# Kernel optimization log

Hardware: AMD Instinct MI355X
Metric: run time of the kernel (lower is better)

Reference implementation:

```python
import jax, jax.numpy as jnp
import numpy as np

F = 128          # num_features
NRBF = 20        # num_rbf_features
N_NODES = 25000
N_EDGES = 400000


def setup_inputs() -> dict:
    key = jax.random.key(0)
    ks = jax.random.split(key, 12)
    inp = {
        "idx_i": jax.random.randint(ks[0], (N_EDGES,), 0, N_NODES, dtype=jnp.int32),
        "idx_j": jax.random.randint(ks[1], (N_EDGES,), 0, N_NODES, dtype=jnp.int32),
        "rel_dir": jax.random.normal(ks[2], (N_EDGES, 3), dtype=jnp.float32),
        "rel_dist_cut": jax.random.uniform(ks[3], (N_EDGES,), dtype=jnp.float32),
        "rbf_features": jax.random.normal(ks[4], (N_EDGES, NRBF), dtype=jnp.float32),
        "scalar_features": jax.random.normal(ks[5], (N_NODES, F), dtype=jnp.float32),
        "vector_features": jax.random.normal(ks[6], (N_NODES, F, 3), dtype=jnp.float32),
        # scalar_network: Linear(F,F) -> SiLU -> Linear(F,3F)
        "W1": jax.random.normal(ks[7], (F, F), dtype=jnp.float32) / np.sqrt(F),
        "b1": jnp.zeros((F,), dtype=jnp.float32),
        "W2": jax.random.normal(ks[8], (3 * F, F), dtype=jnp.float32) / np.sqrt(F),
        "b2": jnp.zeros((3 * F,), dtype=jnp.float32),
        # rbf_network: Linear(NRBF, 3F)
        "Wr": jax.random.normal(ks[9], (3 * F, NRBF), dtype=jnp.float32) / np.sqrt(NRBF),
        "br": jnp.zeros((3 * F,), dtype=jnp.float32),
    }
    return inp


def reference(idx_i, idx_j, rel_dir, rel_dist_cut, rbf_features,
              scalar_features, vector_features, W1, b1, W2, b2, Wr, br):
    n_nodes = scalar_features.shape[0]
    # phi: per-node MLP -> [N, 3F]
    h = jax.nn.silu(scalar_features @ W1.T + b1)
    phi = h @ W2.T + b2
    # W: RBF-derived edge weights gated by cosine-cut distance -> [E, 3F]
    W = (rbf_features @ Wr.T + br) * rel_dist_cut[:, None]
    phi_W = phi[idx_j] * W                                  # [E, 3F]
    phi_W_vv, phi_W_ss, phi_W_vs = jnp.split(phi_W, 3, axis=-1)
    # scatter-add scalar residuals
    scalar_res = jax.ops.segment_sum(phi_W_ss, idx_i, num_segments=n_nodes)
    # per-edge vector messages [E, F, 3]
    vec_per_edge = (vector_features[idx_j] * phi_W_vv[..., None]
                    + phi_W_vs[..., None] * rel_dir[:, None, :])
    vector_res = jax.ops.segment_sum(vec_per_edge, idx_i, num_segments=n_nodes)
    return scalar_features + scalar_res, vector_features + vector_res
```

## Files before the change

### kernel.cpp

```cpp
#include <hip/hip_runtime.h>
#include <hip/hip_fp16.h>

#define F 128
#define F3 384
#define NRBF 20
#define NPB 16
#define CHUNK 64

typedef unsigned int u32;
typedef _Float16 half8 __attribute__((ext_vector_type(8)));
typedef float floatx4 __attribute__((ext_vector_type(4)));

__device__ __forceinline__ float2 uph(u32 u) {
    __half2 h = *(__half2*)&u;
    return __half22float2(h);
}
__device__ __forceinline__ u32 pkh(float a, float b) {
    __half2 h = __floats2half2_rn(a, b);
    return *(u32*)&h;
}

__global__ void prep_kernel(const float* __restrict__ Wr,
                            const float* __restrict__ W1, const float* __restrict__ W2,
                            u32* __restrict__ WrTh, _Float16* __restrict__ Wh,
                            int* __restrict__ counts, int n_nodes) {
    int t = blockIdx.x * blockDim.x + threadIdx.x;
    if (t < 10 * F3) {
        int rr = t / F3, f = t % F3;
        WrTh[rr * F3 + f] = pkh(Wr[f * NRBF + 2 * rr], Wr[f * NRBF + 2 * rr + 1]);
        return;
    }
    int u = t - 10 * F3;
    if (u < (F + F3) * F) {
        int n = u >> 7, k = u & (F - 1);
        float w = (n < F) ? W1[n * F + k] : W2[(size_t)(n - F) * F + k];
        Wh[u] = (_Float16)w;
        return;
    }
    int z = u - (F + F3) * F;
    if (z < n_nodes) counts[z] = 0;
}

__launch_bounds__(256)
__global__ void phi_mfma_kernel(const float* __restrict__ sf,
                                const _Float16* __restrict__ Wh,
                                const float* __restrict__ b1, const float* __restrict__ b2,
                                __half* __restrict__ gbufh, int n_nodes) {
    __shared__ _Float16 hl[4][16][136];
    int tid = threadIdx.x;
    int lane = tid & 63;
    int wv = tid >> 6;
    int col = lane & 15;
    int kg = lane >> 4;
    int row0 = blockIdx.x * 64 + wv * 16;

    half8 a1[4];
#pragma unroll
    for (int kb = 0; kb < 4; kb++) {
        int rr = row0 + col;
        if (rr >= n_nodes) rr = n_nodes - 1;
        const float4* xp = (const float4*)(sf + (size_t)rr * F + kb * 32 + kg * 8);
        float4 x0 = xp[0], x1 = xp[1];
        half8 a;
        a[0] = (_Float16)x0.x; a[1] = (_Float16)x0.y; a[2] = (_Float16)x0.z; a[3] = (_Float16)x0.w;
        a[4] = (_Float16)x1.x; a[5] = (_Float16)x1.y; a[6] = (_Float16)x1.z; a[7] = (_Float16)x1.w;
        a1[kb] = a;
    }

    floatx4 acc[8];
#pragma unroll
    for (int nt = 0; nt < 8; nt++) acc[nt] = (floatx4){0.f, 0.f, 0.f, 0.f};
#pragma unroll
    for (int nt = 0; nt < 8; nt++) {
#pragma unroll
        for (int kb = 0; kb < 4; kb++) {
            half8 b = *(const half8*)(Wh + (size_t)(nt * 16 + col) * F + kb * 32 + kg * 8);
            acc[nt] = __builtin_amdgcn_mfma_f32_16x16x32_f16(a1[kb], b, acc[nt], 0, 0, 0);
        }
    }
#pragma unroll
    for (int nt = 0; nt < 8; nt++) {
        int f1 = nt * 16 + col;
        float bb = b1[f1];
#pragma unroll
        for (int r = 0; r < 4; r++) {
            float v = acc[nt][r] + bb;
            float s = v / (1.f + __expf(-v));
            hl[wv][kg * 4 + r][f1] = (_Float16)s;
        }
    }

    half8 a2[4];
#pragma unroll
    for (int kb = 0; kb < 4; kb++)
        a2[kb] = *(const half8*)&hl[wv][col][kb * 32 + kg * 8];

#pragma unroll
    for (int c = 0; c < 3; c++) {
#pragma unroll
        for (int nt = 0; nt < 8; nt++) acc[nt] = (floatx4){0.f, 0.f, 0.f, 0.f};
#pragma unroll
        for (int nt = 0; nt < 8; nt++) {
#pragma unroll
            for (int kb = 0; kb < 4; kb++) {
                half8 b = *(const half8*)(Wh + (size_t)(F + c * 128 + nt * 16 + col) * F + kb * 32 + kg * 8);
                acc[nt] = __builtin_amdgcn_mfma_f32_16x16x32_f16(a2[kb], b, acc[nt], 0, 0, 0);
            }
        }
#pragma unroll
        for (int nt = 0; nt < 8; nt++) {
            int f2 = c * 128 + nt * 16 + col;
            float bb = b2[f2];
            int slot = (f2 & 63) * 12 + ((f2 >> 6) & 1) * 6 + (f2 >> 7);
#pragma unroll
            for (int r = 0; r < 4; r++) {
                int node = row0 + kg * 4 + r;
                if (node < n_nodes)
                    gbufh[(size_t)node * 768 + slot] = __float2half(acc[nt][r] + bb);
            }
        }
    }
}

__launch_bounds__(256)
__global__ void fusedC_kernel(const int* __restrict__ idx_i, int* __restrict__ counts,
                              const float* __restrict__ vf, __half* __restrict__ gbufh,
                              int n_nodes, int n_edges, int HB) {
    int blk = blockIdx.x, tid = threadIdx.x;
    if (blk < HB) {
        int e = blk * 256 + tid;
        if (e < n_edges) atomicAdd(&counts[idx_i[e]], 1);
    } else {
        int idx = (blk - HB) * 256 + tid;
        int node = idx >> 6, lane = idx & 63;
        if (node < n_nodes) {
            const float* v = vf + (size_t)node * F3;
            __half* g = gbufh + (size_t)node * 768 + lane * 12;
            g[3]  = __float2half(v[lane * 3 + 0]);
            g[4]  = __float2half(v[lane * 3 + 1]);
            g[5]  = __float2half(v[lane * 3 + 2]);
            g[9]  = __float2half(v[(lane + 64) * 3 + 0]);
            g[10] = __float2half(v[(lane + 64) * 3 + 1]);
            g[11] = __float2half(v[(lane + 64) * 3 + 2]);
        }
    }
}

#define SCAN_T 1024
#define SCAN_MAXN 25600
__launch_bounds__(SCAN_T)
__global__ void scan_lds_kernel(const int* __restrict__ counts, int* __restrict__ row_start,
                                int* __restrict__ cursor, int n) {
    __shared__ int sbuf[SCAN_MAXN];
    __shared__ int partial[SCAN_T];
    int t = threadIdx.x;
    for (int i = t; i < n; i += SCAN_T) sbuf[i] = counts[i];
    __syncthreads();
    int C = (n + SCAN_T - 1) / SCAN_T;
    int beg = t * C, end = min(beg + C, n);
    int sum = 0;
    for (int i = beg; i < end; i++) sum += sbuf[i];
    partial[t] = sum;
    __syncthreads();
    for (int off = 1; off < SCAN_T; off <<= 1) {
        int v = (t >= off) ? partial[t - off] : 0;
        __syncthreads();
        partial[t] += v;
        __syncthreads();
    }
    int base = (t == 0) ? 0 : partial[t - 1];
    for (int i = beg; i < end; i++) { int c = sbuf[i]; sbuf[i] = base; base += c; }
    __syncthreads();
    for (int i = t; i < n; i += SCAN_T) { int v = sbuf[i]; row_start[i] = v; cursor[i] = v; }
    if (t == SCAN_T - 1) row_start[n] = partial[SCAN_T - 1];
}

__launch_bounds__(1024)
__global__ void scan_kernel(const int* __restrict__ counts, int* __restrict__ row_start,
                            int* __restrict__ cursor, int n) {
    __shared__ int partial[1024];
    int t = threadIdx.x;
    int C = (n + 1023) / 1024;
    int beg = t * C, end = min(beg + C, n);
    int sum = 0;
    for (int i = beg; i < end; i++) sum += counts[i];
    partial[t] = sum;
    __syncthreads();
    for (int off = 1; off < 1024; off <<= 1) {
        int v = (t >= off) ? partial[t - off] : 0;
        __syncthreads();
        partial[t] += v;
        __syncthreads();
    }
    int base = (t == 0) ? 0 : partial[t - 1];
    for (int i = beg; i < end; i++) {
        int c = counts[i];
        row_start[i] = base; cursor[i] = base; base += c;
    }
    if (t == 1023) row_start[n] = partial[1023];
}

__global__ void build_records(const int* __restrict__ idx_i, const int* __restrict__ idx_j,
                              const float* __restrict__ rel_dir, const float* __restrict__ rdc,
                              const float* __restrict__ rbf, int* __restrict__ cursor,
                              u32* __restrict__ recs, int n_edges) {
    int e = blockIdx.x * blockDim.x + threadIdx.x;
    if (e >= n_edges) return;
    int p = atomicAdd(&cursor[idx_i[e]], 1);
    u32 r[16];
    r[0] = (u32)idx_j[e];
    r[1] = __float_as_uint(rdc[e]);
    r[2] = __float_as_uint(rel_dir[e * 3 + 0]);
    r[3] = __float_as_uint(rel_dir[e * 3 + 1]);
    r[4] = __float_as_uint(rel_dir[e * 3 + 2]);
    const float* rb = rbf + (size_t)e * NRBF;
#pragma unroll
    for (int t = 0; t < 10; t++) r[5 + t] = pkh(rb[2 * t], rb[2 * t + 1]);
    r[15] = 0;
    float4* dst = (float4*)(recs + (size_t)p * 16);
    const float4* src = (const float4*)r;
    dst[0] = src[0]; dst[1] = src[1]; dst[2] = src[2]; dst[3] = src[3];
}

__global__ void scatter_kernel(const int* __restrict__ idx_i, int* __restrict__ cursor,
                               int* __restrict__ edge_order, int n_edges) {
    int e = blockIdx.x * blockDim.x + threadIdx.x;
    if (e < n_edges) {
        int p = atomicAdd(&cursor[idx_i[e]], 1);
        edge_order[p] = e;
    }
}

__launch_bounds__(256)
__global__ void gather4_kernel(const float* __restrict__ sf, const float* __restrict__ vf,
                               const u32* __restrict__ WrTh, const float* __restrict__ br,
                               const u32* __restrict__ gbuf, const u32* __restrict__ recs,
                               const int* __restrict__ row_start,
                               float* __restrict__ out_s, float* __restrict__ out_v,
                               int n_nodes) {
    __shared__ u32 lsm[4][CHUNK * 16];
    int tid = threadIdx.x;
    int lane = tid & 63;
    int wvid = tid >> 6;
    int w = wvid & 1;
    int node = blockIdx.x * 2 + (wvid >> 1);
    if (node >= n_nodes) return;
    u32* lds = lsm[wvid];

    int fb = lane + 64 * w;
    u32 wrpk[3][10];
    float brv[3];
#pragma unroll
    for (int k = 0; k < 3; k++) {
        brv[k] = br[fb + 128 * k];
#pragma unroll
        for (int rr = 0; rr < 10; rr++)
            wrpk[k][rr] = WrTh[rr * F3 + fb + 128 * k];
    }

    float acc_s = 0.f, av0 = 0.f, av1 = 0.f, av2 = 0.f;
    int beg = row_start[node];
    int end = row_start[node + 1];

    for (int cb = beg; cb < end; cb += CHUNK) {
        int cnt = min(CHUNK, end - cb);
        {
            const float4* src = (const float4*)(recs + (size_t)cb * 16);
            int nf4 = cnt * 4;
            for (int t = lane; t < nf4; t += 64)
                ((float4*)lds)[t] = src[t];
        }

        auto issueL = [&](u32& g0, u32& g1, u32& g2, int m) {
            if (m < cnt) {
                int j = (int)lds[m * 16];
                const u32* gp = gbuf + (size_t)j * 384 + lane * 6 + w * 3;
                g0 = gp[0]; g1 = gp[1]; g2 = gp[2];
            }
        };
        auto computeE = [&](u32 g0, u32 g1, u32 g2, int m) {
            const uint4* q = (const uint4*)(lds + m * 16);
            uint4 q0 = q[0], q1 = q[1], q2 = q[2], q3 = q[3];
            float rd = __uint_as_float(q0.y);
            float dx = __uint_as_float(q0.z);
            float dy = __uint_as_float(q0.w);
            float dz = __uint_as_float(q1.x);
            u32 rbu[10] = { q1.y, q1.z, q1.w, q2.x, q2.y, q2.z, q2.w, q3.x, q3.y, q3.z };
            __half2 z2 = __floats2half2_rn(0.f, 0.f);
            __half2 wa0 = z2, wa1 = z2, wa2 = z2;
#pragma unroll
            for (int rr = 0; rr < 10; rr++) {
                __half2 rbh = *(__half2*)&rbu[rr];
                wa0 = __hfma2(rbh, *(__half2*)&wrpk[0][rr], wa0);
                wa1 = __hfma2(rbh, *(__half2*)&wrpk[1][rr], wa1);
                wa2 = __hfma2(rbh, *(__half2*)&wrpk[2][rr], wa2);
            }
            float W0  = __half2float(wa0.x) + __half2float(wa0.y) + brv[0];
            float W1v = __half2float(wa1.x) + __half2float(wa1.y) + brv[1];
            float W2v = __half2float(wa2.x) + __half2float(wa2.y) + brv[2];
            float2 p01  = uph(g0);
            float2 p2v0 = uph(g1);
            float2 v12  = uph(g2);
            float pw0 = W0  * rd * p01.x;
            float pw1 = W1v * rd * p01.y;
            float pw2 = W2v * rd * p2v0.x;
            acc_s += pw1;
            av0 += p2v0.y * pw0 + pw2 * dx;
            av1 += v12.x  * pw0 + pw2 * dy;
            av2 += v12.y  * pw0 + pw2 * dz;
        };

        u32 A0, A1, A2, B0, B1, B2, C0, C1, C2, D0, D1, D2;
        issueL(A0, A1, A2, 0); issueL(B0, B1, B2, 1);
        issueL(C0, C1, C2, 2); issueL(D0, D1, D2, 3);
        int m = 0;
        while (true) {
            if (m >= cnt) break; computeE(A0, A1, A2, m); m++; issueL(A0, A1, A2, m + 3);
            if (m >= cnt) break; computeE(B0, B1, B2, m); m++; issueL(B0, B1, B2, m + 3);
            if (m >= cnt) break; computeE(C0, C1, C2, m); m++; issueL(C0, C1, C2, m + 3);
            if (m >= cnt) break; computeE(D0, D1, D2, m); m++; issueL(D0, D1, D2, m + 3);
        }
    }

    out_s[(size_t)node * F + fb] = sf[(size_t)node * F + fb] + acc_s;
    const float* vfi = vf + (size_t)node * F3 + fb * 3;
    float* ovi = out_v + (size_t)node * F3 + fb * 3;
    ovi[0] = vfi[0] + av0;
    ovi[1] = vfi[1] + av1;
    ovi[2] = vfi[2] + av2;
}

__launch_bounds__(256)
__global__ void gather3_kernel(const int* __restrict__ idx_j,
                               const float* __restrict__ rel_dir, const float* __restrict__ rdc,
                               const float* __restrict__ rbf,
                               const float* __restrict__ sf, const float* __restrict__ vf,
                               const u32* __restrict__ WrTh, const float* __restrict__ br,
                               const u32* __restrict__ gbuf,
                               const int* __restrict__ row_start, const int* __restrict__ edge_order,
                               float* __restrict__ out_s, float* __restrict__ out_v,
                               int n_nodes) {
    int lane = threadIdx.x & 63;
    int w = (threadIdx.x >> 6) & 1;
    int node = blockIdx.x * 2 + (threadIdx.x >> 7);
    if (node >= n_nodes) return;

    int fb = lane + 64 * w;
    u32 wrpk[3][10];
    float brv[3];
#pragma unroll
    for (int k = 0; k < 3; k++) {
        brv[k] = br[fb + 128 * k];
#pragma unroll
        for (int rr = 0; rr < 10; rr++)
            wrpk[k][rr] = WrTh[rr * F3 + fb + 128 * k];
    }

    float acc_s = 0.f, av0 = 0.f, av1 = 0.f, av2 = 0.f;
    int beg = row_start[node];
    int end = row_start[node + 1];

    for (int cb = beg; cb < end; cb += 64) {
        int cnt = min(64, end - cb);
        int jv = 0; float rdv = 0.f, dxv = 0.f, dyv = 0.f, dzv = 0.f;
        u32 rbm[10];
#pragma unroll
        for (int rr = 0; rr < 10; rr++) rbm[rr] = 0;
        if (lane < cnt) {
            int e = edge_order[cb + lane];
            jv = idx_j[e];
            rdv = rdc[e];
            dxv = rel_dir[e * 3 + 0]; dyv = rel_dir[e * 3 + 1]; dzv = rel_dir[e * 3 + 2];
            const float4* rp = (const float4*)(rbf + (size_t)e * NRBF);
            float4 r0 = rp[0], r1 = rp[1], r2 = rp[2], r3 = rp[3], r4 = rp[4];
            rbm[0] = pkh(r0.x, r0.y); rbm[1] = pkh(r0.z, r0.w);
            rbm[2] = pkh(r1.x, r1.y); rbm[3] = pkh(r1.z, r1.w);
            rbm[4] = pkh(r2.x, r2.y); rbm[5] = pkh(r2.z, r2.w);
            rbm[6] = pkh(r3.x, r3.y); rbm[7] = pkh(r3.z, r3.w);
            rbm[8] = pkh(r4.x, r4.y); rbm[9] = pkh(r4.z, r4.w);
        }
        auto issue = [&](u32& g0, u32& g1, u32& g2, int k) {
            int j = __shfl(jv, k, 64);
            const u32* gp = gbuf + (size_t)j * 384 + lane * 6 + w * 3;
            g0 = gp[0]; g1 = gp[1]; g2 = gp[2];
        };
        auto compute = [&](u32 g0, u32 g1, u32 g2, int k) {
            float rd = __shfl(rdv, k, 64);
            float dx = __shfl(dxv, k, 64);
            float dy = __shfl(dyv, k, 64);
            float dz = __shfl(dzv, k, 64);
            __half2 z2 = __floats2half2_rn(0.f, 0.f);
            __half2 wa0 = z2, wa1 = z2, wa2 = z2;
#pragma unroll
            for (int rr = 0; rr < 10; rr++) {
                int rbi = __shfl((int)rbm[rr], k, 64);
                __half2 rbh = *(__half2*)&rbi;
                wa0 = __hfma2(rbh, *(__half2*)&wrpk[0][rr], wa0);
                wa1 = __hfma2(rbh, *(__half2*)&wrpk[1][rr], wa1);
                wa2 = __hfma2(rbh, *(__half2*)&wrpk[2][rr], wa2);
            }
            float W0 = __half2float(wa0.x) + __half2float(wa0.y) + brv[0];
            float W1v = __half2float(wa1.x) + __half2float(wa1.y) + brv[1];
            float W2v = __half2float(wa2.x) + __half2float(wa2.y) + brv[2];
            float2 p01 = uph(g0);
            float2 p2v0 = uph(g1);
            float2 v12 = uph(g2);
            float pw0 = W0 * rd * p01.x;
            float pw1 = W1v * rd * p01.y;
            float pw2 = W2v * rd * p2v0.x;
            acc_s += pw1;
            av0 += p2v0.y * pw0 + pw2 * dx;
            av1 += v12.x  * pw0 + pw2 * dy;
            av2 += v12.y  * pw0 + pw2 * dz;
        };
        u32 A0, A1, A2, B0, B1, B2;
        issue(A0, A1, A2, 0);
        int k = 0;
        while (k + 2 <= cnt) {
            issue(B0, B1, B2, k + 1);
            compute(A0, A1, A2, k);
            if (k + 2 < cnt) issue(A0, A1, A2, k + 2);
            compute(B0, B1, B2, k + 1);
            k += 2;
        }
        if (k < cnt) compute(A0, A1, A2, k);
    }

    out_s[(size_t)node * F + fb] = sf[(size_t)node * F + fb] + acc_s;
    const float* vfi = vf + (size_t)node * F3 + fb * 3;
    float* ovi = out_v + (size_t)node * F3 + fb * 3;
    ovi[0] = vfi[0] + av0;
    ovi[1] = vfi[1] + av1;
    ovi[2] = vfi[2] + av2;
}

__global__ void transpose_wr(const float* __restrict__ Wr, float* __restrict__ WrT) {
    int idx = blockIdx.x * blockDim.x + threadIdx.x;
    if (idx < F3 * NRBF) {
        int f = idx / NRBF, r = idx % NRBF;
        WrT[r * F3 + f] = Wr[idx];
    }
}

__global__ void init_out(const float* __restrict__ sf, const float* __restrict__ vf,
                         float* __restrict__ out, int n_scalar, int n_total) {
    int i = blockIdx.x * blockDim.x + threadIdx.x;
    int n4 = n_total >> 2;
    if (i < n4) {
        float4 v;
        int base = i << 2;
        if (base < n_scalar) v = ((const float4*)sf)[i];
        else                 v = ((const float4*)vf)[i - (n_scalar >> 2)];
        ((float4*)out)[i] = v;
    }
}

__launch_bounds__(256)
__global__ void phi32_kernel(const float* __restrict__ sf,
                             const float* __restrict__ W1, const float* __restrict__ b1,
                             const float* __restrict__ W2, const float* __restrict__ b2,
                             float* __restrict__ phi, int n_nodes) {
    __shared__ float xs[NPB][F];
    __shared__ float hs[NPB][F];
    int tid = threadIdx.x;
    int nb = blockIdx.x * NPB;
    for (int t = tid; t < NPB * F / 4; t += 256) {
        int n  = t / (F / 4);
        int k4 = t % (F / 4);
        float4 v = make_float4(0.f, 0.f, 0.f, 0.f);
        if (nb + n < n_nodes) v = ((const float4*)(sf + (size_t)(nb + n) * F))[k4];
        ((float4*)&xs[n][0])[k4] = v;
    }
    __syncthreads();
    {
        int f = tid & (F - 1);
        int half_ = tid >> 7;
        float acc[8];
#pragma unroll
        for (int nn = 0; nn < 8; nn++) acc[nn] = 0.f;
        const float* w1row = W1 + (size_t)f * F;
        for (int k = 0; k < F; k++) {
            float w = w1row[k];
#pragma unroll
            for (int nn = 0; nn < 8; nn++)
                acc[nn] += xs[half_ * 8 + nn][k] * w;
        }
        float b = b1[f];
#pragma unroll
        for (int nn = 0; nn < 8; nn++) {
            float v = acc[nn] + b;
            hs[half_ * 8 + nn][f] = v / (1.f + __expf(-v));
        }
    }
    __syncthreads();
    for (int f = tid; f < F3; f += 256) {
        float acc[NPB];
#pragma unroll
        for (int n = 0; n < NPB; n++) acc[n] = 0.f;
        const float* w2row = W2 + (size_t)f * F;
        for (int k = 0; k < F; k++) {
            float w = w2row[k];
#pragma unroll
            for (int n = 0; n < NPB; n++)
                acc[n] += hs[n][k] * w;
        }
        float b = b2[f];
        for (int n = 0; n < NPB; n++)
            if (nb + n < n_nodes)
                phi[(size_t)(nb + n) * F3 + f] = acc[n] + b;
    }
}

__launch_bounds__(256)
__global__ void edge_kernel(const int* __restrict__ idx_i, const int* __restrict__ idx_j,
                            const float* __restrict__ rel_dir, const float* __restrict__ rdc,
                            const float* __restrict__ rbf,
                            const float* __restrict__ vf,
                            const float* __restrict__ WrT, const float* __restrict__ br,
                            const float* __restrict__ phi,
                            float* __restrict__ out_s, float* __restrict__ out_v,
                            int n_edges) {
    int lane = threadIdx.x & 63;
    int e = (int)((blockIdx.x * (unsigned)blockDim.x + threadIdx.x) >> 6);
    if (e >= n_edges) return;
    int i = idx_i[e], j = idx_j[e];
    float rd = rdc[e];
    float d0 = rel_dir[e * 3 + 0], d1 = rel_dir[e * 3 + 1], d2 = rel_dir[e * 3 + 2];
    float rb[NRBF];
#pragma unroll
    for (int r = 0; r < NRBF; r++) rb[r] = rbf[(size_t)e * NRBF + r];
    const float* pj = phi + (size_t)j * F3;
    float pw[6];
#pragma unroll
    for (int q = 0; q < 6; q++) {
        int f = lane + 64 * q;
        float acc = br[f];
#pragma unroll
        for (int r = 0; r < NRBF; r++)
            acc += rb[r] * WrT[r * F3 + f];
        pw[q] = acc * rd * pj[f];
    }
    atomicAdd(&out_s[(size_t)i * F + lane],       pw[2]);
    atomicAdd(&out_s[(size_t)i * F + lane + 64],  pw[3]);
    const float* vfj = vf + (size_t)j * F * 3;
    float* ovi = out_v + (size_t)i * F * 3;
#pragma unroll
    for (int h = 0; h < 2; h++) {
        int f = lane + 64 * h;
        float vv = pw[h];
        float vs = pw[4 + h];
        atomicAdd(&ovi[f * 3 + 0], vfj[f * 3 + 0] * vv + vs * d0);
        atomicAdd(&ovi[f * 3 + 1], vfj[f * 3 + 1] * vv + vs * d1);
        atomicAdd(&ovi[f * 3 + 2], vfj[f * 3 + 2] * vv + vs * d2);
    }
}

extern "C" void kernel_launch(void* const* d_in, const int* in_sizes, int n_in,
                              void* d_out, int out_size, void* d_ws, size_t ws_size,
                              hipStream_t stream) {
    const int*   idx_i   = (const int*)d_in[0];
    const int*   idx_j   = (const int*)d_in[1];
    const float* rel_dir = (const float*)d_in[2];
    const float* rdc     = (const float*)d_in[3];
    const float* rbf     = (const float*)d_in[4];
    const float* sf      = (const float*)d_in[5];
    const float* vf      = (const float*)d_in[6];
    const float* W1      = (const float*)d_in[7];
    const float* b1      = (const float*)d_in[8];
    const float* W2      = (const float*)d_in[9];
    const float* b2      = (const float*)d_in[10];
    const float* Wr      = (const float*)d_in[11];
    const float* br      = (const float*)d_in[12];

    int E = in_sizes[0];
    int N = in_sizes[5] / F;

    float* out_s = (float*)d_out;
    float* out_v = out_s + (size_t)N * F;

    size_t off = 0;
    auto slab = [&](size_t bytes) { size_t o = off; off = (off + bytes + 255) & ~(size_t)255; return o; };
    size_t o_wrth = slab((size_t)10 * F3 * sizeof(u32));
    size_t o_wh   = slab((size_t)(F + F3) * F * sizeof(_Float16));
    size_t o_gbuf = slab((size_t)N * 768 * sizeof(__half));
    size_t o_cnt  = slab((size_t)N * sizeof(int));
    size_t o_row  = slab((size_t)(N + 1) * sizeof(int));
    size_t o_rec  = slab((size_t)E * 64);
    size_t need_v5 = off;

    size_t off3 = 0;
    auto slab3 = [&](size_t bytes) { size_t o = off3; off3 = (off3 + bytes + 255) & ~(size_t)255; return o; };
    size_t t_wrth = slab3((size_t)10 * F3 * sizeof(u32));
    size_t t_wh   = slab3((size_t)(F + F3) * F * sizeof(_Float16));
    size_t t_gbuf = slab3((size_t)N * 768 * sizeof(__half));
    size_t t_cnt  = slab3((size_t)N * sizeof(int));
    size_t t_row  = slab3((size_t)(N + 1) * sizeof(int));
    size_t t_ord  = slab3((size_t)E * sizeof(int));
    size_t need_v3 = off3;

    int prep_threads = 10 * F3 + (F + F3) * F + N;
    int HB = (E + 255) / 256;
    int VB = (N + 3) / 4;
    int PHB = (N + 63) / 64;

    if (ws_size >= need_v5) {
        u32*      WrTh      = (u32*)((char*)d_ws + o_wrth);
        _Float16* Wh        = (_Float16*)((char*)d_ws + o_wh);
        __half*   gbufh     = (__half*)((char*)d_ws + o_gbuf);
        u32*      gbuf      = (u32*)gbufh;
        int*      counts    = (int*)((char*)d_ws + o_cnt);
        int*      cursor    = counts;
        int*      row_start = (int*)((char*)d_ws + o_row);
        u32*      recs      = (u32*)((char*)d_ws + o_rec);

        prep_kernel<<<(prep_threads + 255) / 256, 256, 0, stream>>>(Wr, W1, W2, WrTh, Wh, counts, N);
        phi_mfma_kernel<<<PHB, 256, 0, stream>>>(sf, Wh, b1, b2, gbufh, N);
        fusedC_kernel<<<HB + VB, 256, 0, stream>>>(idx_i, counts, vf, gbufh, N, E, HB);
        if (N <= SCAN_MAXN)
            scan_lds_kernel<<<1, SCAN_T, 0, stream>>>(counts, row_start, cursor, N);
        else
            scan_kernel<<<1, 1024, 0, stream>>>(counts, row_start, cursor, N);
        build_records<<<(E + 255) / 256, 256, 0, stream>>>(idx_i, idx_j, rel_dir, rdc, rbf,
                                                           cursor, recs, E);
        gather4_kernel<<<(N + 1) / 2, 256, 0, stream>>>(sf, vf, WrTh, br, gbuf, recs,
                                                        row_start, out_s, out_v, N);
    } else if (ws_size >= need_v3) {
        u32*      WrTh      = (u32*)((char*)d_ws + t_wrth);
        _Float16* Wh        = (_Float16*)((char*)d_ws + t_wh);
        __half*   gbufh     = (__half*)((char*)d_ws + t_gbuf);
        u32*      gbuf      = (u32*)gbufh;
        int*      counts    = (int*)((char*)d_ws + t_cnt);
        int*      cursor    = counts;
        int*      row_start = (int*)((char*)d_ws + t_row);
        int*      edge_ord  = (int*)((char*)d_ws + t_ord);

        prep_kernel<<<(prep_threads + 255) / 256, 256, 0, stream>>>(Wr, W1, W2, WrTh, Wh, counts, N);
        phi_mfma_kernel<<<PHB, 256, 0, stream>>>(sf, Wh, b1, b2, gbufh, N);
        fusedC_kernel<<<HB + VB, 256, 0, stream>>>(idx_i, counts, vf, gbufh, N, E, HB);
        if (N <= SCAN_MAXN)
            scan_lds_kernel<<<1, SCAN_T, 0, stream>>>(counts, row_start, cursor, N);
        else
            scan_kernel<<<1, 1024, 0, stream>>>(counts, row_start, cursor, N);
        scatter_kernel<<<(E + 255) / 256, 256, 0, stream>>>(idx_i, cursor, edge_ord, E);
        gather3_kernel<<<(N + 1) / 2, 256, 0, stream>>>(idx_j, rel_dir, rdc, rbf, sf, vf,
                                                        WrTh, br, gbuf, row_start, edge_ord,
                                                        out_s, out_v, N);
    } else {
        size_t off2 = 0;
        auto slab2 = [&](size_t bytes) { size_t o = off2; off2 = (off2 + bytes + 255) & ~(size_t)255; return o; };
        size_t f_wrt = slab2((size_t)F3 * NRBF * sizeof(float));
        size_t f_phi = slab2((size_t)N * F3 * sizeof(float));
        float* WrT = (float*)((char*)d_ws + f_wrt);
        float* phi = (float*)((char*)d_ws + f_phi);

        int n_scalar = N * F;
        int n_total  = N * F * 4;
        init_out<<<(n_total / 4 + 255) / 256, 256, 0, stream>>>(sf, vf, (float*)d_out, n_scalar, n_total);
        transpose_wr<<<(F3 * NRBF + 255) / 256, 256, 0, stream>>>(Wr, WrT);
        phi32_kernel<<<(N + NPB - 1) / NPB, 256, 0, stream>>>(sf, W1, b1, W2, b2, phi, N);
        edge_kernel<<<(E + 3) / 4, 256, 0, stream>>>(idx_i, idx_j, rel_dir, rdc, rbf,
                                                     vf, WrT, br, phi, out_s, out_v, E);
    }
}
```

Before: 254.8 us.

## Fuse phi MLP, vector-feature packing and edge counting into one kernel; use fdot2

Merges the phi MFMA kernel with the old kernel that counted idx_i and packed vector features. The phi blocks now also convert their own 64 nodes' vector features to half in gbuf, and extra blocks do the count atomics, which removes one launch and its dependency gap. Separately, the per-edge RBF weight dot product now uses fdot2 (half2 inputs, fp32 accumulate) instead of half2 FMA chains with a final reduction. That gives better accuracy and possibly fewer instructions, but the fused phi blocks do more serial work per block.

Result: faster. 233.6 us (-8.3%).

```diff
diff --git a/kernel.cpp b/kernel.cpp
--- a/kernel.cpp
+++ b/kernel.cpp
@@ -18,6 +18,21 @@
 __device__ __forceinline__ u32 pkh(float a, float b) {
     __half2 h = __floats2half2_rn(a, b);
     return *(u32*)&h;
+}
+
+__device__ __forceinline__ float fdot2f(u32 a, u32 b, float c) {
+#if defined(__has_builtin)
+#if __has_builtin(__builtin_amdgcn_fdot2)
+    typedef _Float16 h2 __attribute__((ext_vector_type(2)));
+    return __builtin_amdgcn_fdot2(*(h2*)&a, *(h2*)&b, c, false);
+#else
+    float2 fa = uph(a), fb = uph(b);
+    return fmaf(fa.x, fb.x, fmaf(fa.y, fb.y, c));
+#endif
+#else
+    float2 fa = uph(a), fb = uph(b);
+    return fmaf(fa.x, fb.x, fmaf(fa.y, fb.y, c));
+#endif
 }
 
 __global__ void prep_kernel(const float* __restrict__ Wr,
@@ -42,17 +57,26 @@
 }
 
 __launch_bounds__(256)
-__global__ void phi_mfma_kernel(const float* __restrict__ sf,
-                                const _Float16* __restrict__ Wh,
-                                const float* __restrict__ b1, const float* __restrict__ b2,
-                                __half* __restrict__ gbufh, int n_nodes) {
+__global__ void fusedB2_kernel(const float* __restrict__ sf,
+                               const _Float16* __restrict__ Wh,
+                               const float* __restrict__ b1, const float* __restrict__ b2,
+                               const float* __restrict__ vf, __half* __restrict__ gbufh,
+                               const int* __restrict__ idx_i, int* __restrict__ counts,
+                               int n_nodes, int n_edges, int PHB) {
     __shared__ _Float16 hl[4][16][136];
-    int tid = threadIdx.x;
+    int blk = blockIdx.x, tid = threadIdx.x;
+
+    if (blk >= PHB) {
+        int e = (blk - PHB) * 256 + tid;
+        if (e < n_edges) atomicAdd(&counts[idx_i[e]], 1);
+        return;
+    }
+
     int lane = tid & 63;
     int wv = tid >> 6;
     int col = lane & 15;
     int kg = lane >> 4;
-    int row0 = blockIdx.x * 64 + wv * 16;
+    int row0 = blk * 64 + wv * 16;
 
     half8 a1[4];
 #pragma unroll
@@ -120,28 +144,20 @@
             }
         }
     }
-}
-
-__launch_bounds__(256)
-__global__ void fusedC_kernel(const int* __restrict__ idx_i, int* __restrict__ counts,
-                              const float* __restrict__ vf, __half* __restrict__ gbufh,
-                              int n_nodes, int n_edges, int HB) {
-    int blk = blockIdx.x, tid = threadIdx.x;
-    if (blk < HB) {
-        int e = blk * 256 + tid;
-        if (e < n_edges) atomicAdd(&counts[idx_i[e]], 1);
-    } else {
-        int idx = (blk - HB) * 256 + tid;
-        int node = idx >> 6, lane = idx & 63;
+
+    int base = blk * 64;
+    for (int idx = tid; idx < 64 * 64; idx += 256) {
+        int nl = idx >> 6, ln = idx & 63;
+        int node = base + nl;
         if (node < n_nodes) {
             const float* v = vf + (size_t)node * F3;
-            __half* g = gbufh + (size_t)node * 768 + lane * 12;
-            g[3]  = __float2half(v[lane * 3 + 0]);
-            g[4]  = __float2half(v[lane * 3 + 1]);
-            g[5]  = __float2half(v[lane * 3 + 2]);
-            g[9]  = __float2half(v[(lane + 64) * 3 + 0]);
-            g[10] = __float2half(v[(lane + 64) * 3 + 1]);
-            g[11] = __float2half(v[(lane + 64) * 3 + 2]);
+            u32* gp = (u32*)(gbufh + (size_t)node * 768 + ln * 12);
+            float a0 = v[ln * 3 + 0], a1v = v[ln * 3 + 1], a2v = v[ln * 3 + 2];
+            float c0 = v[(ln + 64) * 3 + 0], c1 = v[(ln + 64) * 3 + 1], c2 = v[(ln + 64) * 3 + 2];
+            ((__half*)gp)[3] = __float2half(a0);
+            gp[2] = pkh(a1v, a2v);
+            ((__half*)gp)[9] = __float2half(c0);
+            gp[5] = pkh(c1, c2);
         }
     }
 }
@@ -232,7 +248,7 @@
 }
 
 __launch_bounds__(256)
-__global__ void gather4_kernel(const float* __restrict__ sf, const float* __restrict__ vf,
+__global__ void gather5_kernel(const float* __restrict__ sf, const float* __restrict__ vf,
                                const u32* __restrict__ WrTh, const float* __restrict__ br,
                                const u32* __restrict__ gbuf, const u32* __restrict__ recs,
                                const int* __restrict__ row_start,
@@ -286,24 +302,19 @@
             float dy = __uint_as_float(q0.w);
             float dz = __uint_as_float(q1.x);
             u32 rbu[10] = { q1.y, q1.z, q1.w, q2.x, q2.y, q2.z, q2.w, q3.x, q3.y, q3.z };
-            __half2 z2 = __floats2half2_rn(0.f, 0.f);
-            __half2 wa0 = z2, wa1 = z2, wa2 = z2;
+            float W0 = brv[0], W1f = brv[1], W2f = brv[2];
 #pragma unroll
             for (int rr = 0; rr < 10; rr++) {
-                __half2 rbh = *(__half2*)&rbu[rr];
-                wa0 = __hfma2(rbh, *(__half2*)&wrpk[0][rr], wa0);
-                wa1 = __hfma2(rbh, *(__half2*)&wrpk[1][rr], wa1);
-                wa2 = __hfma2(rbh, *(__half2*)&wrpk[2][rr], wa2);
+                W0  = fdot2f(rbu[rr], wrpk[0][rr], W0);
+                W1f = fdot2f(rbu[rr], wrpk[1][rr], W1f);
+                W2f = fdot2f(rbu[rr], wrpk[2][rr], W2f);
             }
-            float W0  = __half2float(wa0.x) + __half2float(wa0.y) + brv[0];
-            float W1v = __half2float(wa1.x) + __half2float(wa1.y) + brv[1];
-            float W2v = __half2float(wa2.x) + __half2float(wa2.y) + brv[2];
             float2 p01  = uph(g0);
             float2 p2v0 = uph(g1);
             float2 v12  = uph(g2);
             float pw0 = W0  * rd * p01.x;
-            float pw1 = W1v * rd * p01.y;
-            float pw2 = W2v * rd * p2v0.x;
+            float pw1 = W1f * rd * p01.y;
+            float pw2 = W2f * rd * p2v0.x;
             acc_s += pw1;
             av0 += p2v0.y * pw0 + pw2 * dx;
             av1 += v12.x  * pw0 + pw2 * dy;
@@ -389,25 +400,20 @@
             float dx = __shfl(dxv, k, 64);
             float dy = __shfl(dyv, k, 64);
             float dz = __shfl(dzv, k, 64);
-            __half2 z2 = __floats2half2_rn(0.f, 0.f);
-            __half2 wa0 = z2, wa1 = z2, wa2 = z2;
+            float W0 = brv[0], W1f = brv[1], W2f = brv[2];
 #pragma unroll
             for (int rr = 0; rr < 10; rr++) {
-                int rbi = __shfl((int)rbm[rr], k, 64);
-                __half2 rbh = *(__half2*)&rbi;
-                wa0 = __hfma2(rbh, *(__half2*)&wrpk[0][rr], wa0);
-                wa1 = __hfma2(rbh, *(__half2*)&wrpk[1][rr], wa1);
-                wa2 = __hfma2(rbh, *(__half2*)&wrpk[2][rr], wa2);
+                u32 rbi = (u32)__shfl((int)rbm[rr], k, 64);
+                W0  = fdot2f(rbi, wrpk[0][rr], W0);
+                W1f = fdot2f(rbi, wrpk[1][rr], W1f);
+                W2f = fdot2f(rbi, wrpk[2][rr], W2f);
             }
-            float W0 = __half2float(wa0.x) + __half2float(wa0.y) + brv[0];
-            float W1v = __half2float(wa1.x) + __half2float(wa1.y) + brv[1];
-            float W2v = __half2float(wa2.x) + __half2float(wa2.y) + brv[2];
             float2 p01 = uph(g0);
             float2 p2v0 = uph(g1);
             float2 v12 = uph(g2);
             float pw0 = W0 * rd * p01.x;
-            float pw1 = W1v * rd * p01.y;
-            float pw2 = W2v * rd * p2v0.x;
+            float pw1 = W1f * rd * p01.y;
+            float pw2 = W2f * rd * p2v0.x;
             acc_s += pw1;
             av0 += p2v0.y * pw0 + pw2 * dx;
             av1 += v12.x  * pw0 + pw2 * dy;
@@ -600,7 +606,6 @@
 
     int prep_threads = 10 * F3 + (F + F3) * F + N;
     int HB = (E + 255) / 256;
-    int VB = (N + 3) / 4;
     int PHB = (N + 63) / 64;
 
     if (ws_size >= need_v5) {
@@ -614,15 +619,15 @@
         u32*      recs      = (u32*)((char*)d_ws + o_rec);
 
         prep_kernel<<<(prep_threads + 255) / 256, 256, 0, stream>>>(Wr, W1, W2, WrTh, Wh, counts, N);
-        phi_mfma_kernel<<<PHB, 256, 0, stream>>>(sf, Wh, b1, b2, gbufh, N);
-        fusedC_kernel<<<HB + VB, 256, 0, stream>>>(idx_i, counts, vf, gbufh, N, E, HB);
+        fusedB2_kernel<<<PHB + HB, 256, 0, stream>>>(sf, Wh, b1, b2, vf, gbufh,
+                                                     idx_i, counts, N, E, PHB);
         if (N <= SCAN_MAXN)
             scan_lds_kernel<<<1, SCAN_T, 0, stream>>>(counts, row_start, cursor, N);
         else
             scan_kernel<<<1, 1024, 0, stream>>>(counts, row_start, cursor, N);
         build_records<<<(E + 255) / 256, 256, 0, stream>>>(idx_i, idx_j, rel_dir, rdc, rbf,
                                                            cursor, recs, E);
-        gather4_kernel<<<(N + 1) / 2, 256, 0, stream>>>(sf, vf, WrTh, br, gbuf, recs,
+        gather5_kernel<<<(N + 1) / 2, 256, 0, stream>>>(sf, vf, WrTh, br, gbuf, recs,
                                                         row_start, out_s, out_v, N);
     } else if (ws_size >= need_v3) {
         u32*      WrTh      = (u32*)((char*)d_ws + t_wrth);
@@ -635,8 +640,8 @@
         int*      edge_ord  = (int*)((char*)d_ws + t_ord);
 
         prep_kernel<<<(prep_threads + 255) / 256, 256, 0, stream>>>(Wr, W1, W2, WrTh, Wh, counts, N);
-        phi_mfma_kernel<<<PHB, 256, 0, stream>>>(sf, Wh, b1, b2, gbufh, N);
-        fusedC_kernel<<<HB + VB, 256, 0, stream>>>(idx_i, counts, vf, gbufh, N, E, HB);
+        fusedB2_kernel<<<PHB + HB, 256, 0, stream>>>(sf, Wh, b1, b2, vf, gbufh,
+                                                     idx_i, counts, N, E, PHB);
         if (N <= SCAN_MAXN)
             scan_lds_kernel<<<1, SCAN_T, 0, stream>>>(counts, row_start, cursor, N);
         else
```
